# Optimization experiments

Measured on AMD Instinct MI355X. Metric: run time of the kernel, lower is better.

The kernel has to match this reference:

```python
import jax, jax.numpy as jnp
import numpy as np

PAST, FUT = 64, 16
SB = 2048
N = PAST + FUT  # 80
OUTP = 35       # sum(emb dims) + 3


def _pre(cat, num, emb0, emb1, emb2, W1, b1, W2, b2, W3, b3):
    # pre_processing: embeddings + last-3 numeric cols -> MLP -> concat target col
    e = jnp.concatenate([emb0[cat[:, 0]], emb1[cat[:, 1]], emb2[cat[:, 2]]], -1)
    o = jnp.concatenate([e, num], -1)                 # [n, 35]
    h = jax.nn.relu(o @ W1 + b1)
    h = jax.nn.relu(h @ W2 + b2)
    h = h @ W3 + b3                                   # [n, 34]
    return jnp.concatenate([h, num[:, -1:]], -1)      # [n, 35]


def _gcn(x, src, dst, W, b):
    n = x.shape[0]
    h = x @ W
    deg = 1.0 + jax.ops.segment_sum(jnp.ones(src.shape, x.dtype), dst, num_segments=n)
    dinv = jax.lax.rsqrt(deg)
    msg = h[src] * (dinv[src] * dinv[dst])[:, None]
    agg = jax.ops.segment_sum(msg, dst, num_segments=n) + h * (dinv * dinv)[:, None]
    return agg + b


def _forward(x1_cat, x1_num, x2_cat, x2_num, e1, e2,
             emb0, emb1, emb2, pW1, pb1, pW2, pb2, pW3, pb3,
             g1W1, g1b1, g1W2, g1b2, g2W1, g2b1, g2W2, g2b2,
             kerW, smoothing, M):
    # masked-softmax adjacency A = softmax(relu(M M^T) masked to lower-tri, axis=1)
    Araw = jax.nn.relu(M @ M.T)
    tril = jnp.tril(jnp.ones((N, N), Araw.dtype))
    A = jax.nn.softmax(jnp.where(tril == 0, -jnp.inf, Araw), axis=1)

    x = _pre(x1_cat, x1_num, emb0, emb1, emb2, pW1, pb1, pW2, pb2, pW3, pb3)   # [SB*PAST, 35]
    x2 = _pre(x2_cat, x2_num, emb0, emb1, emb2, pW1, pb1, pW2, pb2, pW3, pb3)
    x2 = x2.reshape(SB, FUT, OUTP)

    # gnn1: GCN(35->64) -> ReLU -> GCN(64->34)
    h = jax.nn.relu(_gcn(x, e1[0], e1[1], g1W1, g1b1))
    x1 = _gcn(h, e1[0], e1[1], g1W2, g1b2).reshape(SB, PAST, OUTP - 1)

    x_kernel = jnp.concatenate([x1, x2[:, :, :-1]], -2)        # [SB, N, 34]
    y_kernel = x.reshape(SB, PAST, OUTP)[:, :, -1:]            # [SB, PAST, 1]

    # Mahalanobis kernel attention
    theta = kerW @ kerW.T
    theta = (theta + theta.T) / 2
    x_p = x_kernel[:, :PAST, :]
    x_f = x_kernel[:, PAST:, :]
    diff = x_p[:, None, :, :] - x_f[:, :, None, :]             # [SB, FUT, PAST, 34]
    # diagonal of diff @ theta @ diff^T, computed directly
    alpha = jnp.einsum('bqpo,oO,bqpO->bqp', diff, theta, diff)
    alpha = -0.5 * alpha / (jax.nn.sigmoid(smoothing[0]) * 0.01)
    A_tmp = A[PAST:, :PAST]                                    # [FUT, PAST]
    alpha = jnp.where(A_tmp[None] == 0, -jnp.inf, alpha)
    alpha = jax.nn.softmax(alpha, -1)
    yh = jnp.einsum('bqp,bpo->bqo', alpha, y_kernel)           # [SB, FUT, 1]

    x2 = jnp.concatenate([x2[:, :, :-1], yh], -1)              # [SB, FUT, 35]
    # gnn2: GCN(35->64) -> ReLU -> GCN(64->1)
    h2 = jax.nn.relu(_gcn(x2.reshape(-1, OUTP), e2[0], e2[1], g2W1, g2b1))
    out = _gcn(h2, e2[0], e2[1], g2W2, g2b2).reshape(SB, FUT)

    # cdist over concatenated past+future features, via norm trick
    xa = jnp.concatenate([x.reshape(SB, PAST, OUTP), x2], -2)  # [SB, N, 35]
    sq = jnp.sum(xa * xa, -1)
    d2 = sq[:, :, None] + sq[:, None, :] - 2.0 * jnp.einsum('bnd,bmd->bnm', xa, xa)
    cd = jnp.sqrt(jnp.maximum(d2, 0.0))
    return out, cd, A


def setup_inputs():
    key = jax.random.key(0)
    ks = jax.random.split(key, 24)
    f32 = jnp.float32
    n1, n2 = SB * PAST, SB * FUT
    E1, E2 = n1 * 8, n2 * 8
    return {
        'x1_cat': jax.random.randint(ks[0], (n1, 3), 0, 7, dtype=jnp.int32),
        'x1_num': jax.random.normal(ks[1], (n1, 3), f32),
        'x2_cat': jax.random.randint(ks[2], (n2, 3), 0, 7, dtype=jnp.int32),
        'x2_num': jax.random.normal(ks[3], (n2, 3), f32),
        'edge_index1': jax.random.randint(ks[4], (2, E1), 0, n1, dtype=jnp.int32),
        'edge_index2': jax.random.randint(ks[5], (2, E2), 0, n2, dtype=jnp.int32),
        'emb0': jax.random.normal(ks[6], (24, 16), f32),
        'emb1': jax.random.normal(ks[7], (7, 8), f32),
        'emb2': jax.random.normal(ks[8], (12, 8), f32),
        'pre_W1': jax.random.normal(ks[9], (35, 128), f32) * 0.1,
        'pre_b1': jnp.zeros((128,), f32),
        'pre_W2': jax.random.normal(ks[10], (128, 128), f32) * 0.08,
        'pre_b2': jnp.zeros((128,), f32),
        'pre_W3': jax.random.normal(ks[11], (128, 34), f32) * 0.08,
        'pre_b3': jnp.zeros((34,), f32),
        'g1_W1': jax.random.normal(ks[12], (35, 64), f32) * 0.1,
        'g1_b1': jnp.zeros((64,), f32),
        'g1_W2': jax.random.normal(ks[13], (64, 34), f32) * 0.1,
        'g1_b2': jnp.zeros((34,), f32),
        'g2_W1': jax.random.normal(ks[14], (35, 64), f32) * 0.1,
        'g2_b1': jnp.zeros((64,), f32),
        'g2_W2': jax.random.normal(ks[15], (64, 1), f32) * 0.1,
        'g2_b2': jnp.zeros((1,), f32),
        'ker_W': jax.random.normal(ks[16], (34, 128), f32) * 0.1,
        'smoothing': jax.random.normal(ks[17], (1,), f32),
        'M': jax.random.normal(ks[18], (N, N // 3), f32) * 0.1,
    }


def reference(x1_cat, x1_num, x2_cat, x2_num, edge_index1, edge_index2,
              emb0, emb1, emb2, pre_W1, pre_b1, pre_W2, pre_b2, pre_W3, pre_b3,
              g1_W1, g1_b1, g1_W2, g1_b2, g2_W1, g2_b1, g2_W2, g2_b2,
              ker_W, smoothing, M):
    return _forward(x1_cat, x1_num, x2_cat, x2_num, edge_index1, edge_index2,
                    emb0, emb1, emb2, pre_W1, pre_b1, pre_W2, pre_b2, pre_W3, pre_b3,
                    g1_W1, g1_b1, g1_W2, g1_b2, g2_W1, g2_b1, g2_W2, g2_b2,
                    ker_W, smoothing, M)
```

## Files before the change

### kernel.cpp

```cpp
#include <hip/hip_runtime.h>
#include <math.h>

#define PASTN 64
#define FUTN 16
#define NN 80

typedef __attribute__((ext_vector_type(8))) short sh8;
typedef __attribute__((ext_vector_type(4))) float f32x4;

__device__ __forceinline__ unsigned short f2bf(float f) {
    unsigned int u = __float_as_uint(f);
    return (unsigned short)((u + 0x7FFFu + ((u >> 16) & 1u)) >> 16);
}
__device__ __forceinline__ float bf2f(unsigned short s) {
    return __uint_as_float(((unsigned int)s) << 16);
}

__global__ __launch_bounds__(256) void k_setup(const float* __restrict__ M, const float* __restrict__ kerW,
                                               const float* __restrict__ smoothing,
                                               float* __restrict__ A_ws, float* __restrict__ A_out,
                                               float* __restrict__ theta, float* __restrict__ scale)
{
    __shared__ float Ms[80 * 26];
    __shared__ float Ar[80 * 80];
    const int t = threadIdx.x;
    for (int i = t; i < 80 * 26; i += 256) Ms[i] = M[i];
    __syncthreads();
    for (int idx = t; idx < 6400; idx += 256) {
        int i = idx / 80, j = idx - 80 * i;
        float acc = 0.f;
#pragma unroll
        for (int k = 0; k < 26; ++k) acc = fmaf(Ms[i * 26 + k], Ms[j * 26 + k], acc);
        Ar[idx] = fmaxf(acc, 0.f);
    }
    __syncthreads();
    if (t < 80) {
        float mx = -1e30f;
        for (int j = 0; j <= t; ++j) mx = fmaxf(mx, Ar[t * 80 + j]);
        float s = 0.f;
        for (int j = 0; j <= t; ++j) s += expf(Ar[t * 80 + j] - mx);
        float inv = 1.f / s;
        for (int j = 0; j < 80; ++j) {
            float v = (j <= t) ? expf(Ar[t * 80 + j] - mx) * inv : 0.f;
            A_ws[t * 80 + j] = v;
            A_out[t * 80 + j] = v;
        }
    }
    for (int idx = t; idx < 34 * 34; idx += 256) {
        int i = idx / 34, j = idx - 34 * i;
        float acc = 0.f;
        for (int k = 0; k < 128; ++k) acc = fmaf(kerW[i * 128 + k], kerW[j * 128 + k], acc);
        theta[idx] = acc;
    }
    if (t == 0) {
        float s0 = smoothing[0];
        float sig = 1.f / (1.f + expf(-s0));
        scale[0] = -0.5f / (sig * 0.01f);
    }
}

__global__ void k_wconv(const float* __restrict__ W2, unsigned short* __restrict__ Wh,
                        unsigned short* __restrict__ Wl)
{
    int g = blockIdx.x * 256 + threadIdx.x;
    int i = g & 7, ln = (g >> 3) & 63, ks = (g >> 9) & 3, nt = g >> 11;
    int col = nt * 16 + (ln & 15);
    int k = ks * 32 + ((ln >> 4) << 3) + i;
    float w = W2[k * 128 + col];
    unsigned short hi = f2bf(w);
    Wh[g] = hi;
    Wl[g] = f2bf(w - bf2f(hi));
}

__global__ void k_deg2(const int* __restrict__ dst1, const int* __restrict__ dst2,
                       int* __restrict__ deg1, int* __restrict__ deg2,
                       int E1, int E2, int nbe1)
{
    int gb = blockIdx.x;
    if (gb < nbe1) {
        int e = gb * 256 + threadIdx.x;
        if (e < E1) atomicAdd(&deg1[dst1[e]], 1);
    } else {
        int e = (gb - nbe1) * 256 + threadIdx.x;
        if (e < E2) atomicAdd(&deg2[dst2[e]], 1);
    }
}

#define SCHUNK 1024
__global__ __launch_bounds__(256) void k_scan_reduce2(const int* __restrict__ deg1, const int* __restrict__ deg2,
                                                      int* __restrict__ bsumA, int* __restrict__ bsumB,
                                                      int n1, int n2, int nb1)
{
    __shared__ int sd[256];
    const int gb = blockIdx.x, t = threadIdx.x;
    const int which = (gb < nb1) ? 0 : 1;
    const int b = which ? gb - nb1 : gb;
    const int* deg = which ? deg2 : deg1;
    const int n = which ? n2 : n1;
    const int base = b * SCHUNK;
    int s = 0;
#pragma unroll
    for (int j = 0; j < 4; ++j) {
        int i = base + t + j * 256;
        if (i < n) s += deg[i];
    }
    sd[t] = s;
    __syncthreads();
    for (int o = 128; o > 0; o >>= 1) {
        if (t < o) sd[t] += sd[t + o];
        __syncthreads();
    }
    if (t == 0) (which ? bsumB : bsumA)[b] = sd[0];
}

__global__ __launch_bounds__(1024) void k_scan_mid2(int* __restrict__ bsumA, int* __restrict__ bsumB,
                                                    int nbA, int nbB)
{
    __shared__ int sd[1024];
    const int t = threadIdx.x;
    int* bsum = (blockIdx.x == 0) ? bsumA : bsumB;
    int nb = (blockIdx.x == 0) ? nbA : nbB;
    int orig = (t < nb) ? bsum[t] : 0;
    sd[t] = orig;
    __syncthreads();
    for (int o = 1; o < 1024; o <<= 1) {
        int v = (t >= o) ? sd[t - o] : 0;
        __syncthreads();
        sd[t] += v;
        __syncthreads();
    }
    if (t < nb) bsum[t] = sd[t] - orig;
}

__global__ __launch_bounds__(256) void k_scan_final2(const int* __restrict__ deg1, const int* __restrict__ deg2,
                                                     const int* __restrict__ bsumA, const int* __restrict__ bsumB,
                                                     int* __restrict__ rs1, int* __restrict__ rs2,
                                                     int* __restrict__ cur1, int* __restrict__ cur2,
                                                     float* __restrict__ dinv1, float* __restrict__ dinv2,
                                                     int n1, int n2, int nb1)
{
    __shared__ int sd[256];
    const int gb = blockIdx.x, t = threadIdx.x;
    const int which = (gb < nb1) ? 0 : 1;
    const int b = which ? gb - nb1 : gb;
    const int* deg = which ? deg2 : deg1;
    const int* bsum = which ? bsumB : bsumA;
    int* rs = which ? rs2 : rs1;
    int* cur = which ? cur2 : cur1;
    float* dinv = which ? dinv2 : dinv1;
    const int n = which ? n2 : n1;
    const int base = b * SCHUNK + t * 4;
    int v0 = (base + 0 < n) ? deg[base + 0] : 0;
    int v1 = (base + 1 < n) ? deg[base + 1] : 0;
    int v2 = (base + 2 < n) ? deg[base + 2] : 0;
    int v3 = (base + 3 < n) ? deg[base + 3] : 0;
    int tsum = v0 + v1 + v2 + v3;
    sd[t] = tsum;
    __syncthreads();
    int incl = tsum;
    for (int o = 1; o < 256; o <<= 1) {
        int v = (t >= o) ? sd[t - o] : 0;
        __syncthreads();
        incl += v;
        sd[t] = incl;
        __syncthreads();
    }
    int off = bsum[b] + incl - tsum;
    if (base + 0 < n) { rs[base + 0] = off;            cur[base + 0] = off;            dinv[base + 0] = rsqrtf(1.f + (float)v0); }
    if (base + 1 < n) { rs[base + 1] = off + v0;       cur[base + 1] = off + v0;       dinv[base + 1] = rsqrtf(1.f + (float)v1); }
    if (base + 2 < n) { rs[base + 2] = off + v0 + v1;  cur[base + 2] = off + v0 + v1;  dinv[base + 2] = rsqrtf(1.f + (float)v2); }
    if (base + 3 < n) { rs[base + 3] = off + v0 + v1 + v2; cur[base + 3] = off + v0 + v1 + v2; dinv[base + 3] = rsqrtf(1.f + (float)v3); }
}

__global__ void k_fill2(const int* __restrict__ src1, const int* __restrict__ dst1,
                        const int* __restrict__ src2, const int* __restrict__ dst2,
                        int* __restrict__ cur1, int* __restrict__ cur2,
                        int* __restrict__ out1, int* __restrict__ out2,
                        int E1, int E2, int nbe1)
{
    int gb = blockIdx.x;
    if (gb < nbe1) {
        int e = gb * 256 + threadIdx.x;
        if (e < E1) { int pos = atomicAdd(&cur1[dst1[e]], 1); out1[pos] = src1[e]; }
    } else {
        int e = (gb - nbe1) * 256 + threadIdx.x;
        if (e < E2) { int pos = atomicAdd(&cur2[dst2[e]], 1); out2[pos] = src2[e]; }
    }
}

template <int DIN>
__global__ __launch_bounds__(256) void k_gcn_s(const int* __restrict__ rs, const int* __restrict__ deg,
                                               const int* __restrict__ srcs, const float* __restrict__ dinv,
                                               const float* __restrict__ Hs, const float* __restrict__ W,
                                               const float* __restrict__ b, float* __restrict__ Out, int n)
{
    const int w = threadIdx.x >> 6, lane = threadIdx.x & 63;
    const int row = blockIdx.x * 4 + w;
    __shared__ float ag[4][DIN];
    const float di = dinv[row];
    const int e0 = rs[row];
    const int d = deg[row];
    float acc = (lane < DIN) ? Hs[(size_t)row * DIN + lane] : 0.f;
    int e = 0;
    for (; e + 8 <= d; e += 8) {
        int s0 = srcs[e0 + e + 0], s1 = srcs[e0 + e + 1], s2 = srcs[e0 + e + 2], s3 = srcs[e0 + e + 3];
        int s4 = srcs[e0 + e + 4], s5 = srcs[e0 + e + 5], s6 = srcs[e0 + e + 6], s7 = srcs[e0 + e + 7];
        float h0 = 0.f, h1 = 0.f, h2 = 0.f, h3 = 0.f, h4 = 0.f, h5 = 0.f, h6 = 0.f, h7 = 0.f;
        if (lane < DIN) {
            h0 = Hs[(size_t)s0 * DIN + lane]; h1 = Hs[(size_t)s1 * DIN + lane];
            h2 = Hs[(size_t)s2 * DIN + lane]; h3 = Hs[(size_t)s3 * DIN + lane];
            h4 = Hs[(size_t)s4 * DIN + lane]; h5 = Hs[(size_t)s5 * DIN + lane];
            h6 = Hs[(size_t)s6 * DIN + lane]; h7 = Hs[(size_t)s7 * DIN + lane];
        }
        acc += ((h0 + h1) + (h2 + h3)) + ((h4 + h5) + (h6 + h7));
    }
    for (; e + 4 <= d; e += 4) {
        int s0 = srcs[e0 + e + 0], s1 = srcs[e0 + e + 1], s2 = srcs[e0 + e + 2], s3 = srcs[e0 + e + 3];
        float h0 = 0.f, h1 = 0.f, h2 = 0.f, h3 = 0.f;
        if (lane < DIN) {
            h0 = Hs[(size_t)s0 * DIN + lane]; h1 = Hs[(size_t)s1 * DIN + lane];
            h2 = Hs[(size_t)s2 * DIN + lane]; h3 = Hs[(size_t)s3 * DIN + lane];
        }
        acc += (h0 + h1) + (h2 + h3);
    }
    for (; e < d; ++e) {
        int s = srcs[e0 + e];
        if (lane < DIN) acc += Hs[(size_t)s * DIN + lane];
    }
    if (lane < DIN) ag[w][lane] = acc;
    __syncthreads();
    float o = 0.f;
#pragma unroll
    for (int i = 0; i < DIN; ++i) o = fmaf(ag[w][i], W[i * 64 + lane], o);
    Out[(size_t)row * 64 + lane] = fmaxf(fmaf(di, o, b[lane]), 0.f);
}

template <int D>
__global__ __launch_bounds__(256) void k_pcomb_s(const int* __restrict__ rs, const int* __restrict__ deg,
                                                 const int* __restrict__ srcs, const float* __restrict__ dinv,
                                                 const float* __restrict__ Hs, const float* __restrict__ b,
                                                 float* __restrict__ dest, int n)
{
    const int wid = (blockIdx.x * blockDim.x + threadIdx.x) >> 6;
    const int lane = threadIdx.x & 63;
    if (wid >= n) return;
    const float di = dinv[wid];
    const int e0 = rs[wid];
    const int d = deg[wid];
    float acc = (lane < D) ? Hs[(size_t)wid * D + lane] : 0.f;
    int e = 0;
    for (; e + 8 <= d; e += 8) {
        int s0 = srcs[e0 + e + 0], s1 = srcs[e0 + e + 1], s2 = srcs[e0 + e + 2], s3 = srcs[e0 + e + 3];
        int s4 = srcs[e0 + e + 4], s5 = srcs[e0 + e + 5], s6 = srcs[e0 + e + 6], s7 = srcs[e0 + e + 7];
        float h0 = 0.f, h1 = 0.f, h2 = 0.f, h3 = 0.f, h4 = 0.f, h5 = 0.f, h6 = 0.f, h7 = 0.f;
        if (lane < D) {
            h0 = Hs[(size_t)s0 * D + lane]; h1 = Hs[(size_t)s1 * D + lane];
            h2 = Hs[(size_t)s2 * D + lane]; h3 = Hs[(size_t)s3 * D + lane];
            h4 = Hs[(size_t)s4 * D + lane]; h5 = Hs[(size_t)s5 * D + lane];
            h6 = Hs[(size_t)s6 * D + lane]; h7 = Hs[(size_t)s7 * D + lane];
        }
        acc += ((h0 + h1) + (h2 + h3)) + ((h4 + h5) + (h6 + h7));
    }
    for (; e + 4 <= d; e += 4) {
        int s0 = srcs[e0 + e + 0], s1 = srcs[e0 + e + 1], s2 = srcs[e0 + e + 2], s3 = srcs[e0 + e + 3];
        float h0 = 0.f, h1 = 0.f, h2 = 0.f, h3 = 0.f;
        if (lane < D) {
            h0 = Hs[(size_t)s0 * D + lane]; h1 = Hs[(size_t)s1 * D + lane];
            h2 = Hs[(size_t)s2 * D + lane]; h3 = Hs[(size_t)s3 * D + lane];
        }
        acc += (h0 + h1) + (h2 + h3);
    }
    for (; e < d; ++e) {
        int s = srcs[e0 + e];
        if (lane < D) acc += Hs[(size_t)s * D + lane];
    }
    if (lane < D) dest[(size_t)wid * D + lane] = fmaf(di, acc, b[lane]);
}

__global__ void k_pcomb1_s(const int* __restrict__ rs, const int* __restrict__ deg,
                           const int* __restrict__ srcs, const float* __restrict__ dinv,
                           const float* __restrict__ Hs, const float* __restrict__ b,
                           float* __restrict__ dest, int n)
{
    int r = blockIdx.x * blockDim.x + threadIdx.x;
    if (r >= n) return;
    int e0 = rs[r], d = deg[r];
    float acc = Hs[r];
    int e = 0;
    for (; e + 8 <= d; e += 8) {
        acc += ((Hs[srcs[e0 + e + 0]] + Hs[srcs[e0 + e + 1]]) + (Hs[srcs[e0 + e + 2]] + Hs[srcs[e0 + e + 3]]))
             + ((Hs[srcs[e0 + e + 4]] + Hs[srcs[e0 + e + 5]]) + (Hs[srcs[e0 + e + 6]] + Hs[srcs[e0 + e + 7]]));
    }
    for (; e + 4 <= d; e += 4) {
        acc += (Hs[srcs[e0 + e + 0]] + Hs[srcs[e0 + e + 1]]) + (Hs[srcs[e0 + e + 2]] + Hs[srcs[e0 + e + 3]]);
    }
    for (; e < d; ++e) acc += Hs[srcs[e0 + e]];
    dest[r] = fmaf(dinv[r], acc, b[0]);
}

#define PR 32
__global__ __launch_bounds__(256) void k_pre_all(const int* __restrict__ cat1, const float* __restrict__ num1,
                                                 const int* __restrict__ cat2, const float* __restrict__ num2,
                                                 const float* __restrict__ emb0, const float* __restrict__ emb1,
                                                 const float* __restrict__ emb2,
                                                 const float* __restrict__ W1, const float* __restrict__ b1,
                                                 const unsigned short* __restrict__ W2fh,
                                                 const unsigned short* __restrict__ W2fl,
                                                 const float* __restrict__ b2,
                                                 const float* __restrict__ W3, const float* __restrict__ b3,
                                                 const float* __restrict__ dinv1, const float* __restrict__ dinv2,
                                                 float* __restrict__ X1, float* __restrict__ Xs1,
                                                 float* __restrict__ X2, float* __restrict__ Xs2,
                                                 int nblk1)
{
    __shared__ float ldsB[128 * 32];
    __shared__ __align__(16) unsigned short h1h[128 * 32];
    __shared__ __align__(16) unsigned short h1l[128 * 32];
    float* oT = ldsB;
    float* h2T = ldsB;
    const int t = threadIdx.x;
    const int ct = t & 31;
    const int rg = t >> 5;
    const int gb = blockIdx.x;
    const int g2 = (gb >= nblk1);
    const int* cat = g2 ? cat2 : cat1;
    const float* num = g2 ? num2 : num1;
    const float* dinv = g2 ? dinv2 : dinv1;
    float* X = g2 ? X2 : X1;
    float* Xs = g2 ? Xs2 : Xs1;
    const int base = (g2 ? gb - nblk1 : gb) * PR;

    for (int idx = t; idx < 35 * PR; idx += 256) {
        int i = idx >> 5, r = idx & 31;
        int row = base + r;
        float v;
        if (i < 16) v = emb0[cat[row * 3 + 0] * 16 + i];
        else if (i < 24) v = emb1[cat[row * 3 + 1] * 8 + (i - 16)];
        else if (i < 32) v = emb2[cat[row * 3 + 2] * 8 + (i - 24)];
        else v = num[row * 3 + (i - 32)];
        oT[i * PR + (((r >> 2) ^ (i & 7)) << 2) + (r & 3)] = v;
    }
    __syncthreads();

    {
        float acc[4][4];
        float4 bb = *(const float4*)(b1 + 4 * ct);
        const float bbv[4] = {bb.x, bb.y, bb.z, bb.w};
#pragma unroll
        for (int c = 0; c < 4; ++c)
#pragma unroll
            for (int r = 0; r < 4; ++r) acc[c][r] = bbv[c];
        for (int i = 0; i < 35; ++i) {
            float4 ov = *(const float4*)(oT + i * PR + ((rg ^ (i & 7)) << 2));
            float4 wv = *(const float4*)(W1 + i * 128 + 4 * ct);
            const float o4[4] = {ov.x, ov.y, ov.z, ov.w};
            const float w4[4] = {wv.x, wv.y, wv.z, wv.w};
#pragma unroll
            for (int c = 0; c < 4; ++c)
#pragma unroll
                for (int r = 0; r < 4; ++r) acc[c][r] = fmaf(w4[c], o4[r], acc[c][r]);
        }
#pragma unroll
        for (int j = 0; j < 4; ++j) {
            int row32 = 4 * rg + j;
            int rowm = row32 & 15;
            int off = row32 * 128 + ((((ct >> 1) ^ rowm)) << 3) + ((ct & 1) << 2);
            ushort4 hi4, lo4;
            float h0 = fmaxf(acc[0][j], 0.f);
            float h1v = fmaxf(acc[1][j], 0.f);
            float h2v = fmaxf(acc[2][j], 0.f);
            float h3v = fmaxf(acc[3][j], 0.f);
            hi4.x = f2bf(h0); lo4.x = f2bf(h0 - bf2f(hi4.x));
            hi4.y = f2bf(h1v); lo4.y = f2bf(h1v - bf2f(hi4.y));
            hi4.z = f2bf(h2v); lo4.z = f2bf(h2v - bf2f(hi4.z));
            hi4.w = f2bf(h3v); lo4.w = f2bf(h3v - bf2f(hi4.w));
            *(ushort4*)(h1h + off) = hi4;
            *(ushort4*)(h1l + off) = lo4;
        }
    }
    __syncthreads();

    {
        const int wv = t >> 6, ln = t & 63;
        const int mt = wv & 1, ng = wv >> 1;
        const int lr = ln & 15, lh = ln >> 4;
        f32x4 acc[4];
#pragma unroll
        for (int j = 0; j < 4; ++j) acc[j] = (f32x4){0.f, 0.f, 0.f, 0.f};
        const int arow = (mt * 16 + lr) * 128;
#pragma unroll
        for (int ks = 0; ks < 4; ++ks) {
            const int sc = (((ks * 4 + lh) ^ lr) << 3);
            sh8 ahi = *(const sh8*)(h1h + arow + sc);
            sh8 alo = *(const sh8*)(h1l + arow + sc);
#pragma unroll
            for (int j = 0; j < 4; ++j) {
                const int fbase = ((((ng * 4 + j) * 4 + ks) * 64 + ln) << 3);
                sh8 bhi = *(const sh8*)(W2fh + fbase);
                sh8 blo = *(const sh8*)(W2fl + fbase);
                acc[j] = __builtin_amdgcn_mfma_f32_16x16x32_bf16(ahi, bhi, acc[j], 0, 0, 0);
                acc[j] = __builtin_amdgcn_mfma_f32_16x16x32_bf16(ahi, blo, acc[j], 0, 0, 0);
                acc[j] = __builtin_amdgcn_mfma_f32_16x16x32_bf16(alo, bhi, acc[j], 0, 0, 0);
            }
        }
        __syncthreads();
#pragma unroll
        for (int j = 0; j < 4; ++j) {
            int col = (ng * 4 + j) * 16 + lr;
            int rg3 = mt * 4 + lh;
            float bc = b2[col];
            float4 v;
            v.x = fmaxf(acc[j][0] + bc, 0.f);
            v.y = fmaxf(acc[j][1] + bc, 0.f);
            v.z = fmaxf(acc[j][2] + bc, 0.f);
            v.w = fmaxf(acc[j][3] + bc, 0.f);
            *(float4*)(h2T + col * PR + ((rg3 ^ (col & 7)) << 2)) = v;
        }
    }
    __syncthreads();

    for (int task = t; task < 34 * 8; task += 256) {
        int j = task >> 3, rg3 = task & 7;
        float a0 = b3[j], a1 = a0, a2 = a0, a3 = a0;
#pragma unroll 4
        for (int k = 0; k < 128; ++k) {
            float4 hv = *(const float4*)(h2T + k * PR + ((rg3 ^ (k & 7)) << 2));
            float wv = W3[k * 34 + j];
            a0 = fmaf(hv.x, wv, a0);
            a1 = fmaf(hv.y, wv, a1);
            a2 = fmaf(hv.z, wv, a2);
            a3 = fmaf(hv.w, wv, a3);
        }
        size_t rb = (size_t)(base + rg3 * 4);
        float d0 = dinv[rb + 0], d1 = dinv[rb + 1], d2 = dinv[rb + 2], d3 = dinv[rb + 3];
        X[(rb + 0) * 35 + j] = a0;  Xs[(rb + 0) * 35 + j] = a0 * d0;
        X[(rb + 1) * 35 + j] = a1;  Xs[(rb + 1) * 35 + j] = a1 * d1;
        X[(rb + 2) * 35 + j] = a2;  Xs[(rb + 2) * 35 + j] = a2 * d2;
        X[(rb + 3) * 35 + j] = a3;  Xs[(rb + 3) * 35 + j] = a3 * d3;
    }
    if (t < PR) {
        int row = base + t;
        float v = num[row * 3 + 2];
        X[(size_t)row * 35 + 34] = v;
        Xs[(size_t)row * 35 + 34] = v * dinv[row];
    }
}

template <int DIN, int DOUT, bool BIAS, bool RELU, bool SCALE>
__global__ void k_gemm(const float* __restrict__ Xin, int ldin, const float* __restrict__ W,
                       const float* __restrict__ b, const float* __restrict__ oscale,
                       float* __restrict__ Out, int n)
{
    __shared__ float Ws[DIN * DOUT];
    for (int i = threadIdx.x; i < DIN * DOUT; i += blockDim.x) Ws[i] = W[i];
    __syncthreads();
    int idx = blockIdx.x * blockDim.x + threadIdx.x;
    if (idx >= n * DOUT) return;
    int row = idx / DOUT, j = idx - row * DOUT;
    const float4* xr4 = (const float4*)(Xin + (size_t)row * ldin);
    float acc = BIAS ? b[j] : 0.f;
#pragma unroll
    for (int i4 = 0; i4 < DIN / 4; ++i4) {
        float4 x = xr4[i4];
        acc = fmaf(x.x, Ws[(4 * i4 + 0) * DOUT + j], acc);
        acc = fmaf(x.y, Ws[(4 * i4 + 1) * DOUT + j], acc);
        acc = fmaf(x.z, Ws[(4 * i4 + 2) * DOUT + j], acc);
        acc = fmaf(x.w, Ws[(4 * i4 + 3) * DOUT + j], acc);
    }
    if (RELU) acc = fmaxf(acc, 0.f);
    if (SCALE) acc *= oscale[row];
    Out[idx] = acc;
}

__global__ __launch_bounds__(256) void k_alpha(const float* __restrict__ X1,
                                               const float* __restrict__ X,
                                               float* __restrict__ X2,
                                               float* __restrict__ Xs2,
                                               const float* __restrict__ dinv2,
                                               const float* __restrict__ theta,
                                               const float* __restrict__ A,
                                               const float* __restrict__ scale)
{
    const int b = blockIdx.x;
    const int t = threadIdx.x;
    const int p = t & 63;
    const int w = t >> 6;
    __shared__ float th[34 * 34];
    __shared__ float xpS[64 * 35];
    __shared__ float xfS[16 * 34];
    __shared__ float UfS[16 * 34];
    __shared__ float upPart[4][64];
    __shared__ float upS[64];
    __shared__ float yS[64];

    for (int i = t; i < 34 * 34; i += 256) th[i] = theta[i];
    for (int i = t; i < 64 * 34; i += 256) {
        int r = i / 34, o = i - 34 * r;
        xpS[r * 35 + o] = X1[(size_t)(b * 64 + r) * 34 + o];
    }
    for (int i = t; i < 16 * 34; i += 256) {
        int q = i / 34, o = i - 34 * q;
        xfS[i] = X2[(size_t)(b * 16 + q) * 35 + o];
    }
    if (t < 64) yS[t] = X[(size_t)(b * 64 + t) * 35 + 34];
    __syncthreads();

    for (int i = t; i < 16 * 34; i += 256) {
        int q = i / 34, o = i - 34 * q;
        float a = 0.f;
#pragma unroll
        for (int O = 0; O < 34; ++O) a = fmaf(th[o * 34 + O], xfS[q * 34 + O], a);
        UfS[i] = a;
    }
    {
        const int o0 = w * 9;
        const int o1 = (o0 + 9 < 34) ? o0 + 9 : 34;
        float a = 0.f;
        for (int o = o0; o < o1; ++o) {
            float s2 = 0.f;
#pragma unroll
            for (int O = 0; O < 34; ++O) s2 = fmaf(th[o * 34 + O], xpS[p * 35 + O], s2);
            a = fmaf(xpS[p * 35 + o], s2, a);
        }
        upPart[w][p] = a;
    }
    __syncthreads();
    if (t < 64) upS[t] = upPart[0][t] + upPart[1][t] + upPart[2][t] + upPart[3][t];
    __syncthreads();

    const float sc = scale[0];
    const float up = upS[p];
    const float y = yS[p];
#pragma unroll
    for (int i = 0; i < 4; ++i) {
        const int q = w + 4 * i;
        float g = 0.f;
#pragma unroll
        for (int o = 0; o < 34; ++o) g = fmaf(UfS[q * 34 + o], xpS[p * 35 + o], g);
        float a = sc * (up - 2.f * g);
        if (A[(PASTN + q) * NN + p] == 0.f) a = -INFINITY;
        float mx = a;
#pragma unroll
        for (int off = 32; off > 0; off >>= 1) mx = fmaxf(mx, __shfl_xor(mx, off));
        float e = expf(a - mx);
        float s = e;
#pragma unroll
        for (int off = 32; off > 0; off >>= 1) s += __shfl_xor(s, off);
        float c = (e / s) * y;
#pragma unroll
        for (int off = 32; off > 0; off >>= 1) c += __shfl_xor(c, off);
        if (p == 0) {
            size_t ridx = (size_t)(b * 16 + q);
            X2[ridx * 35 + 34] = c;
            Xs2[ridx * 35 + 34] = c * dinv2[ridx];
        }
    }
}

__global__ __launch_bounds__(256) void k_cd(const float* __restrict__ X, const float* __restrict__ X2,
                                            float* __restrict__ cd)
{
    const int b = blockIdx.x;
    const int t = threadIdx.x;
    __shared__ float xa[80 * 44];
    __shared__ float sq[80];
    for (int idx = t; idx < 80 * 44; idx += 256) {
        int nrow = idx / 44, k = idx - 44 * nrow;
        float v = 0.f;
        if (k < 35)
            v = (nrow < 64) ? X[(size_t)(b * 64 + nrow) * 35 + k]
                            : X2[(size_t)(b * 16 + (nrow - 64)) * 35 + k];
        xa[idx] = v;
    }
    __syncthreads();
    const float4* xa4 = (const float4*)xa;
    if (t < 80) {
        float acc = 0.f;
#pragma unroll
        for (int c = 0; c < 9; ++c) {
            float4 v = xa4[t * 11 + c];
            acc = fmaf(v.x, v.x, fmaf(v.y, v.y, fmaf(v.z, v.z, fmaf(v.w, v.w, acc))));
        }
        sq[t] = acc;
    }
    __syncthreads();
    const int ti = t >> 4;
    const int tj = t & 15;
    float dot[5][5];
#pragma unroll
    for (int r = 0; r < 5; ++r)
#pragma unroll
        for (int c = 0; c < 5; ++c) dot[r][c] = 0.f;
#pragma unroll
    for (int ch = 0; ch < 9; ++ch) {
        float4 av[5], bv[5];
#pragma unroll
        for (int r = 0; r < 5; ++r) av[r] = xa4[(5 * ti + r) * 11 + ch];
#pragma unroll
        for (int c = 0; c < 5; ++c) bv[c] = xa4[(5 * tj + c) * 11 + ch];
#pragma unroll
        for (int r = 0; r < 5; ++r)
#pragma unroll
            for (int c = 0; c < 5; ++c)
                dot[r][c] = fmaf(av[r].x, bv[c].x, fmaf(av[r].y, bv[c].y,
                              fmaf(av[r].z, bv[c].z, fmaf(av[r].w, bv[c].w, dot[r][c]))));
    }
    float* out = cd + (size_t)b * 6400;
#pragma unroll
    for (int r = 0; r < 5; ++r) {
        int n_ = 5 * ti + r;
        float sn = sq[n_];
#pragma unroll
        for (int c = 0; c < 5; ++c) {
            int m = 5 * tj + c;
            float d2 = sn + sq[m] - 2.f * dot[r][c];
            out[n_ * 80 + m] = sqrtf(fmaxf(d2, 0.f));
        }
    }
}

extern "C" void kernel_launch(void* const* d_in, const int* in_sizes, int n_in,
                              void* d_out, int out_size, void* d_ws, size_t ws_size,
                              hipStream_t stream)
{
    const int* x1_cat = (const int*)d_in[0];
    const float* x1_num = (const float*)d_in[1];
    const int* x2_cat = (const int*)d_in[2];
    const float* x2_num = (const float*)d_in[3];
    const int* e1 = (const int*)d_in[4];
    const int* e2 = (const int*)d_in[5];
    const float* emb0 = (const float*)d_in[6];
    const float* emb1 = (const float*)d_in[7];
    const float* emb2 = (const float*)d_in[8];
    const float* pW1 = (const float*)d_in[9];
    const float* pb1 = (const float*)d_in[10];
    const float* pW2 = (const float*)d_in[11];
    const float* pb2 = (const float*)d_in[12];
    const float* pW3 = (const float*)d_in[13];
    const float* pb3 = (const float*)d_in[14];
    const float* g1W1 = (const float*)d_in[15];
    const float* g1b1 = (const float*)d_in[16];
    const float* g1W2 = (const float*)d_in[17];
    const float* g1b2 = (const float*)d_in[18];
    const float* g2W1 = (const float*)d_in[19];
    const float* g2b1 = (const float*)d_in[20];
    const float* g2W2 = (const float*)d_in[21];
    const float* g2b2 = (const float*)d_in[22];
    const float* kerW = (const float*)d_in[23];
    const float* smoothing = (const float*)d_in[24];
    const float* M = (const float*)d_in[25];

    const int n1 = in_sizes[0] / 3;
    const int n2 = in_sizes[2] / 3;
    const int E1 = in_sizes[4] / 2;
    const int E2 = in_sizes[5] / 2;
    const int SBc = n2 / FUTN;

    float* w = (float*)d_ws;
    size_t off = 0;
    float* scale = w + off; off += 16;
    float* theta = w + off; off += 1184;
    float* Aws = w + off; off += 6400;
    float* X = w + off; off += (size_t)n1 * 35;
    float* Xs1 = w + off; off += (size_t)n1 * 35;
    float* X2 = w + off; off += (size_t)n2 * 35;
    float* Xs2 = w + off; off += (size_t)n2 * 35;
    float* dinv1 = w + off; off += (size_t)n1;
    float* dinv2 = w + off; off += (size_t)n2;
    float* B2 = w + off; off += (size_t)n1 * 64;
    float* B3 = w + off; off += (size_t)n1 * 34;
    float* B4 = w + off; off += (size_t)n1 * 34;
    off = (off + 3) & ~(size_t)3;
    unsigned short* W2fh = (unsigned short*)(w + off); off += 8192;
    unsigned short* W2fl = (unsigned short*)(w + off); off += 8192;
    int* iw = (int*)(w + off);
    size_t ioff = 0;
    int* degi1 = iw + ioff; ioff += n1;
    int* degi2 = iw + ioff; ioff += n2;
    int* rs1 = iw + ioff; ioff += n1;
    int* cur1 = iw + ioff; ioff += n1;
    int* srcs1 = iw + ioff; ioff += E1;
    int* rs2 = iw + ioff; ioff += n2;
    int* cur2 = iw + ioff; ioff += n2;
    int* srcs2 = iw + ioff; ioff += E2;
    int* bsumA = iw + ioff; ioff += 1024;
    int* bsumB = iw + ioff; ioff += 1024;

    float* out_f = (float*)d_out;
    float* cd_f = out_f + (size_t)SBc * FUTN;
    float* A_out = cd_f + (size_t)SBc * NN * NN;

    auto cdiv = [](long long a, long long b) { return (unsigned)((a + b - 1) / b); };

    hipMemsetAsync(degi1, 0, ((size_t)n1 + n2) * 4, stream);
    k_setup<<<1, 256, 0, stream>>>(M, kerW, smoothing, Aws, A_out, theta, scale);
    k_wconv<<<64, 256, 0, stream>>>(pW2, W2fh, W2fl);

    const int nbe1 = cdiv(E1, 256), nbe2 = cdiv(E2, 256);
    k_deg2<<<nbe1 + nbe2, 256, 0, stream>>>(e1 + E1, e2 + E2, degi1, degi2, E1, E2, nbe1);

    const int nb1 = cdiv(n1, SCHUNK), nb2 = cdiv(n2, SCHUNK);
    k_scan_reduce2<<<nb1 + nb2, 256, 0, stream>>>(degi1, degi2, bsumA, bsumB, n1, n2, nb1);
    k_scan_mid2<<<2, 1024, 0, stream>>>(bsumA, bsumB, nb1, nb2);
    k_scan_final2<<<nb1 + nb2, 256, 0, stream>>>(degi1, degi2, bsumA, bsumB, rs1, rs2, cur1, cur2,
                                                 dinv1, dinv2, n1, n2, nb1);
    k_fill2<<<nbe1 + nbe2, 256, 0, stream>>>(e1, e1 + E1, e2, e2 + E2, cur1, cur2, srcs1, srcs2, E1, E2, nbe1);

    k_pre_all<<<n1 / PR + n2 / PR, 256, 0, stream>>>(x1_cat, x1_num, x2_cat, x2_num,
                                                     emb0, emb1, emb2, pW1, pb1, W2fh, W2fl, pb2, pW3, pb3,
                                                     dinv1, dinv2, X, Xs1, X2, Xs2, n1 / PR);

    k_gcn_s<35><<<cdiv(n1, 4), 256, 0, stream>>>(rs1, degi1, srcs1, dinv1, Xs1, g1W1, g1b1, B2, n1);

    k_gemm<64, 34, false, false, true><<<cdiv((long long)n1 * 34, 256), 256, 0, stream>>>(B2, 64, g1W2, nullptr, dinv1, B3, n1);
    k_pcomb_s<34><<<cdiv(n1, 4), 256, 0, stream>>>(rs1, degi1, srcs1, dinv1, B3, g1b2, B4, n1);

    k_alpha<<<SBc, 256, 0, stream>>>(B4, X, X2, Xs2, dinv2, theta, Aws, scale);

    k_gcn_s<35><<<cdiv(n2, 4), 256, 0, stream>>>(rs2, degi2, srcs2, dinv2, Xs2, g2W1, g2b1, B2, n2);

    k_gemm<64, 1, false, false, true><<<cdiv(n2, 256), 256, 0, stream>>>(B2, 64, g2W2, nullptr, dinv2, B3, n2);
    k_pcomb1_s<<<cdiv(n2, 256), 256, 0, stream>>>(rs2, degi2, srcs2, dinv2, B3, g2b2, out_f, n2);

    k_cd<<<SBc, 256, 0, stream>>>(X, X2, cd_f);
}
```

Measured before the change: 710.0 us.

## Move pre-processing MLP layers 1 and 3 onto split-bf16 MFMA

The first and third layers of the pre-processing MLP move from scalar FP32 FMA loops onto bf16 MFMA, using the same hi/lo split-bf16 (three-product) scheme already used for layer 2. The weight-conversion kernel now pre-packs W1 (K padded to 64) and W3 (N padded to 48) into MFMA fragment layout. LDS buffers are unified into swizzled hi/lo bf16 tiles shared across the three stages. This trades FP32 ALU work for matrix-core work plus conversion overhead, and the split-bf16 approximation slightly reduces accuracy.

```diff
diff --git a/kernel.cpp b/kernel.cpp
--- a/kernel.cpp
+++ b/kernel.cpp
@@ -59,17 +59,41 @@
     }
 }
 
-__global__ void k_wconv(const float* __restrict__ W2, unsigned short* __restrict__ Wh,
-                        unsigned short* __restrict__ Wl)
+__global__ void k_wconv(const float* __restrict__ W1, const float* __restrict__ W2,
+                        const float* __restrict__ W3,
+                        unsigned short* __restrict__ W1h, unsigned short* __restrict__ W1l,
+                        unsigned short* __restrict__ W2h, unsigned short* __restrict__ W2l,
+                        unsigned short* __restrict__ W3h, unsigned short* __restrict__ W3l)
 {
     int g = blockIdx.x * 256 + threadIdx.x;
-    int i = g & 7, ln = (g >> 3) & 63, ks = (g >> 9) & 3, nt = g >> 11;
-    int col = nt * 16 + (ln & 15);
-    int k = ks * 32 + ((ln >> 4) << 3) + i;
-    float w = W2[k * 128 + col];
+    float w;
+    unsigned short *dh, *dl;
+    int gi;
+    if (g < 8192) {
+        gi = g;
+        int i = gi & 7, l = (gi >> 3) & 63, ks = (gi >> 9) & 1, nt = gi >> 10;
+        int col = nt * 16 + (l & 15);
+        int k = ks * 32 + ((l >> 4) << 3) + i;
+        w = (k < 35) ? W1[k * 128 + col] : 0.f;
+        dh = W1h; dl = W1l;
+    } else if (g < 24576) {
+        gi = g - 8192;
+        int i = gi & 7, l = (gi >> 3) & 63, ks = (gi >> 9) & 3, nt = gi >> 11;
+        int col = nt * 16 + (l & 15);
+        int k = ks * 32 + ((l >> 4) << 3) + i;
+        w = W2[k * 128 + col];
+        dh = W2h; dl = W2l;
+    } else {
+        gi = g - 24576;
+        int i = gi & 7, l = (gi >> 3) & 63, ks = (gi >> 9) & 3, nt = gi >> 11;
+        int col = nt * 16 + (l & 15);
+        int k = ks * 32 + ((l >> 4) << 3) + i;
+        w = (col < 34) ? W3[k * 34 + col] : 0.f;
+        dh = W3h; dl = W3l;
+    }
     unsigned short hi = f2bf(w);
-    Wh[g] = hi;
-    Wl[g] = f2bf(w - bf2f(hi));
+    dh[gi] = hi;
+    dl[gi] = f2bf(w - bf2f(hi));
 }
 
 __global__ void k_deg2(const int* __restrict__ dst1, const int* __restrict__ dst2,
@@ -303,24 +327,23 @@
                                                  const int* __restrict__ cat2, const float* __restrict__ num2,
                                                  const float* __restrict__ emb0, const float* __restrict__ emb1,
                                                  const float* __restrict__ emb2,
-                                                 const float* __restrict__ W1, const float* __restrict__ b1,
-                                                 const unsigned short* __restrict__ W2fh,
-                                                 const unsigned short* __restrict__ W2fl,
+                                                 const unsigned short* __restrict__ W1h, const unsigned short* __restrict__ W1l,
+                                                 const float* __restrict__ b1,
+                                                 const unsigned short* __restrict__ W2h, const unsigned short* __restrict__ W2l,
                                                  const float* __restrict__ b2,
-                                                 const float* __restrict__ W3, const float* __restrict__ b3,
+                                                 const unsigned short* __restrict__ W3h, const unsigned short* __restrict__ W3l,
+                                                 const float* __restrict__ b3,
                                                  const float* __restrict__ dinv1, const float* __restrict__ dinv2,
                                                  float* __restrict__ X1, float* __restrict__ Xs1,
                                                  float* __restrict__ X2, float* __restrict__ Xs2,
                                                  int nblk1)
 {
-    __shared__ float ldsB[128 * 32];
-    __shared__ __align__(16) unsigned short h1h[128 * 32];
-    __shared__ __align__(16) unsigned short h1l[128 * 32];
-    float* oT = ldsB;
-    float* h2T = ldsB;
+    __shared__ __align__(16) unsigned short bufh[32 * 128];
+    __shared__ __align__(16) unsigned short bufl[32 * 128];
     const int t = threadIdx.x;
-    const int ct = t & 31;
-    const int rg = t >> 5;
+    const int wv = t >> 6, ln = t & 63;
+    const int mt = wv & 1, wg = wv >> 1;
+    const int lr = ln & 15, lh = ln >> 4;
     const int gb = blockIdx.x;
     const int g2 = (gb >= nblk1);
     const int* cat = g2 ? cat2 : cat1;
@@ -330,113 +353,141 @@
     float* Xs = g2 ? Xs2 : Xs1;
     const int base = (g2 ? gb - nblk1 : gb) * PR;
 
-    for (int idx = t; idx < 35 * PR; idx += 256) {
-        int i = idx >> 5, r = idx & 31;
-        int row = base + r;
-        float v;
-        if (i < 16) v = emb0[cat[row * 3 + 0] * 16 + i];
-        else if (i < 24) v = emb1[cat[row * 3 + 1] * 8 + (i - 16)];
-        else if (i < 32) v = emb2[cat[row * 3 + 2] * 8 + (i - 24)];
-        else v = num[row * 3 + (i - 32)];
-        oT[i * PR + (((r >> 2) ^ (i & 7)) << 2) + (r & 3)] = v;
-    }
-    __syncthreads();
-
+    for (int idx = t; idx < 32 * 64; idx += 256) {
+        int r = idx >> 6, k = idx & 63;
+        float v = 0.f;
+        if (k < 16) v = emb0[cat[(base + r) * 3 + 0] * 16 + k];
+        else if (k < 24) v = emb1[cat[(base + r) * 3 + 1] * 8 + (k - 16)];
+        else if (k < 32) v = emb2[cat[(base + r) * 3 + 2] * 8 + (k - 24)];
+        else if (k < 35) v = num[(base + r) * 3 + (k - 32)];
+        unsigned short hi = f2bf(v);
+        int ho = r * 64 + (((k >> 3) ^ (r & 7)) << 3) + (k & 7);
+        bufh[ho] = hi;
+        bufl[ho] = f2bf(v - bf2f(hi));
+    }
+    __syncthreads();
+
+    f32x4 a1[4];
     {
-        float acc[4][4];
-        float4 bb = *(const float4*)(b1 + 4 * ct);
-        const float bbv[4] = {bb.x, bb.y, bb.z, bb.w};
-#pragma unroll
-        for (int c = 0; c < 4; ++c)
-#pragma unroll
-            for (int r = 0; r < 4; ++r) acc[c][r] = bbv[c];
-        for (int i = 0; i < 35; ++i) {
-            float4 ov = *(const float4*)(oT + i * PR + ((rg ^ (i & 7)) << 2));
-            float4 wv = *(const float4*)(W1 + i * 128 + 4 * ct);
-            const float o4[4] = {ov.x, ov.y, ov.z, ov.w};
-            const float w4[4] = {wv.x, wv.y, wv.z, wv.w};
-#pragma unroll
-            for (int c = 0; c < 4; ++c)
-#pragma unroll
-                for (int r = 0; r < 4; ++r) acc[c][r] = fmaf(w4[c], o4[r], acc[c][r]);
+        const int ra = mt * 16 + lr;
+        sh8 ah[2], al[2];
+#pragma unroll
+        for (int ks = 0; ks < 2; ++ks) {
+            int off = ra * 64 + ((((ks * 4 + lh)) ^ (ra & 7)) << 3);
+            ah[ks] = *(const sh8*)(bufh + off);
+            al[ks] = *(const sh8*)(bufl + off);
         }
 #pragma unroll
         for (int j = 0; j < 4; ++j) {
-            int row32 = 4 * rg + j;
-            int rowm = row32 & 15;
-            int off = row32 * 128 + ((((ct >> 1) ^ rowm)) << 3) + ((ct & 1) << 2);
-            ushort4 hi4, lo4;
-            float h0 = fmaxf(acc[0][j], 0.f);
-            float h1v = fmaxf(acc[1][j], 0.f);
-            float h2v = fmaxf(acc[2][j], 0.f);
-            float h3v = fmaxf(acc[3][j], 0.f);
-            hi4.x = f2bf(h0); lo4.x = f2bf(h0 - bf2f(hi4.x));
-            hi4.y = f2bf(h1v); lo4.y = f2bf(h1v - bf2f(hi4.y));
-            hi4.z = f2bf(h2v); lo4.z = f2bf(h2v - bf2f(hi4.z));
-            hi4.w = f2bf(h3v); lo4.w = f2bf(h3v - bf2f(hi4.w));
-            *(ushort4*)(h1h + off) = hi4;
-            *(ushort4*)(h1l + off) = lo4;
-        }
-    }
-    __syncthreads();
-
+            const int nt = wg + 2 * j;
+            f32x4 acc = (f32x4){0.f, 0.f, 0.f, 0.f};
+#pragma unroll
+            for (int ks = 0; ks < 2; ++ks) {
+                const int fb = (((nt * 2 + ks) * 64 + ln) << 3);
+                sh8 bh = *(const sh8*)(W1h + fb);
+                sh8 bl = *(const sh8*)(W1l + fb);
+                acc = __builtin_amdgcn_mfma_f32_16x16x32_bf16(ah[ks], bh, acc, 0, 0, 0);
+                acc = __builtin_amdgcn_mfma_f32_16x16x32_bf16(ah[ks], bl, acc, 0, 0, 0);
+                acc = __builtin_amdgcn_mfma_f32_16x16x32_bf16(al[ks], bh, acc, 0, 0, 0);
+            }
+            a1[j] = acc;
+        }
+    }
+    __syncthreads();
+#pragma unroll
+    for (int j = 0; j < 4; ++j) {
+        const int f = (wg + 2 * j) * 16 + lr;
+        const float bb = b1[f];
+#pragma unroll
+        for (int reg = 0; reg < 4; ++reg) {
+            const int row = mt * 16 + lh * 4 + reg;
+            float v = fmaxf(a1[j][reg] + bb, 0.f);
+            unsigned short hi = f2bf(v);
+            int ho = row * 128 + ((((f >> 3)) ^ (row & 15)) << 3) + (f & 7);
+            bufh[ho] = hi;
+            bufl[ho] = f2bf(v - bf2f(hi));
+        }
+    }
+    __syncthreads();
+
+    f32x4 a2[4];
+#pragma unroll
+    for (int j = 0; j < 4; ++j) a2[j] = (f32x4){0.f, 0.f, 0.f, 0.f};
     {
-        const int wv = t >> 6, ln = t & 63;
-        const int mt = wv & 1, ng = wv >> 1;
-        const int lr = ln & 15, lh = ln >> 4;
-        f32x4 acc[4];
-#pragma unroll
-        for (int j = 0; j < 4; ++j) acc[j] = (f32x4){0.f, 0.f, 0.f, 0.f};
-        const int arow = (mt * 16 + lr) * 128;
+        const int ra = mt * 16 + lr;
 #pragma unroll
         for (int ks = 0; ks < 4; ++ks) {
-            const int sc = (((ks * 4 + lh) ^ lr) << 3);
-            sh8 ahi = *(const sh8*)(h1h + arow + sc);
-            sh8 alo = *(const sh8*)(h1l + arow + sc);
+            int off = ra * 128 + (((ks * 4 + lh) ^ lr) << 3);
+            sh8 ah = *(const sh8*)(bufh + off);
+            sh8 al = *(const sh8*)(bufl + off);
 #pragma unroll
             for (int j = 0; j < 4; ++j) {
-                const int fbase = ((((ng * 4 + j) * 4 + ks) * 64 + ln) << 3);
-                sh8 bhi = *(const sh8*)(W2fh + fbase);
-                sh8 blo = *(const sh8*)(W2fl + fbase);
-                acc[j] = __builtin_amdgcn_mfma_f32_16x16x32_bf16(ahi, bhi, acc[j], 0, 0, 0);
-                acc[j] = __builtin_amdgcn_mfma_f32_16x16x32_bf16(ahi, blo, acc[j], 0, 0, 0);
-                acc[j] = __builtin_amdgcn_mfma_f32_16x16x32_bf16(alo, bhi, acc[j], 0, 0, 0);
+                const int nt = wg * 4 + j;
+                const int fb = (((nt * 4 + ks) * 64 + ln) << 3);
+                sh8 bh = *(const sh8*)(W2h + fb);
+                sh8 bl = *(const sh8*)(W2l + fb);
+                a2[j] = __builtin_amdgcn_mfma_f32_16x16x32_bf16(ah, bh, a2[j], 0, 0, 0);
+                a2[j] = __builtin_amdgcn_mfma_f32_16x16x32_bf16(ah, bl, a2[j], 0, 0, 0);
+                a2[j] = __builtin_amdgcn_mfma_f32_16x16x32_bf16(al, bh, a2[j], 0, 0, 0);
             }
         }
-        __syncthreads();
-#pragma unroll
-        for (int j = 0; j < 4; ++j) {
-            int col = (ng * 4 + j) * 16 + lr;
-            int rg3 = mt * 4 + lh;
-            float bc = b2[col];
-            float4 v;
-            v.x = fmaxf(acc[j][0] + bc, 0.f);
-            v.y = fmaxf(acc[j][1] + bc, 0.f);
-            v.z = fmaxf(acc[j][2] + bc, 0.f);
-            v.w = fmaxf(acc[j][3] + bc, 0.f);
-            *(float4*)(h2T + col * PR + ((rg3 ^ (col & 7)) << 2)) = v;
-        }
-    }
-    __syncthreads();
-
-    for (int task = t; task < 34 * 8; task += 256) {
-        int j = task >> 3, rg3 = task & 7;
-        float a0 = b3[j], a1 = a0, a2 = a0, a3 = a0;
-#pragma unroll 4
-        for (int k = 0; k < 128; ++k) {
-            float4 hv = *(const float4*)(h2T + k * PR + ((rg3 ^ (k & 7)) << 2));
-            float wv = W3[k * 34 + j];
-            a0 = fmaf(hv.x, wv, a0);
-            a1 = fmaf(hv.y, wv, a1);
-            a2 = fmaf(hv.z, wv, a2);
-            a3 = fmaf(hv.w, wv, a3);
-        }
-        size_t rb = (size_t)(base + rg3 * 4);
-        float d0 = dinv[rb + 0], d1 = dinv[rb + 1], d2 = dinv[rb + 2], d3 = dinv[rb + 3];
-        X[(rb + 0) * 35 + j] = a0;  Xs[(rb + 0) * 35 + j] = a0 * d0;
-        X[(rb + 1) * 35 + j] = a1;  Xs[(rb + 1) * 35 + j] = a1 * d1;
-        X[(rb + 2) * 35 + j] = a2;  Xs[(rb + 2) * 35 + j] = a2 * d2;
-        X[(rb + 3) * 35 + j] = a3;  Xs[(rb + 3) * 35 + j] = a3 * d3;
+    }
+    __syncthreads();
+#pragma unroll
+    for (int j = 0; j < 4; ++j) {
+        const int f = (wg * 4 + j) * 16 + lr;
+        const float bb = b2[f];
+#pragma unroll
+        for (int reg = 0; reg < 4; ++reg) {
+            const int row = mt * 16 + lh * 4 + reg;
+            float v = fmaxf(a2[j][reg] + bb, 0.f);
+            unsigned short hi = f2bf(v);
+            int ho = row * 128 + ((((f >> 3)) ^ (row & 15)) << 3) + (f & 7);
+            bufh[ho] = hi;
+            bufl[ho] = f2bf(v - bf2f(hi));
+        }
+    }
+    __syncthreads();
+
+    f32x4 a3[2];
+    a3[0] = (f32x4){0.f, 0.f, 0.f, 0.f};
+    a3[1] = (f32x4){0.f, 0.f, 0.f, 0.f};
+    {
+        const int ra = mt * 16 + lr;
+#pragma unroll
+        for (int ks = 0; ks < 4; ++ks) {
+            int off = ra * 128 + (((ks * 4 + lh) ^ lr) << 3);
+            sh8 ah = *(const sh8*)(bufh + off);
+            sh8 al = *(const sh8*)(bufl + off);
+#pragma unroll
+            for (int j = 0; j < 2; ++j) {
+                const int nt = wg * 2 + j;
+                if (nt >= 3) continue;
+                const int fb = (((nt * 4 + ks) * 64 + ln) << 3);
+                sh8 bh = *(const sh8*)(W3h + fb);
+                sh8 bl = *(const sh8*)(W3l + fb);
+                a3[j] = __builtin_amdgcn_mfma_f32_16x16x32_bf16(ah, bh, a3[j], 0, 0, 0);
+                a3[j] = __builtin_amdgcn_mfma_f32_16x16x32_bf16(ah, bl, a3[j], 0, 0, 0);
+                a3[j] = __builtin_amdgcn_mfma_f32_16x16x32_bf16(al, bh, a3[j], 0, 0, 0);
+            }
+        }
+    }
+#pragma unroll
+    for (int j = 0; j < 2; ++j) {
+        const int nt = wg * 2 + j;
+        if (nt >= 3) continue;
+        const int jc = nt * 16 + lr;
+        if (jc < 34) {
+            const float bb = b3[jc];
+#pragma unroll
+            for (int reg = 0; reg < 4; ++reg) {
+                const int row = mt * 16 + lh * 4 + reg;
+                const int gr = base + row;
+                float v = a3[j][reg] + bb;
+                X[(size_t)gr * 35 + jc] = v;
+                Xs[(size_t)gr * 35 + jc] = v * dinv[gr];
+            }
+        }
     }
     if (t < PR) {
         int row = base + t;
@@ -671,8 +722,12 @@
     float* B3 = w + off; off += (size_t)n1 * 34;
     float* B4 = w + off; off += (size_t)n1 * 34;
     off = (off + 3) & ~(size_t)3;
+    unsigned short* W1fh = (unsigned short*)(w + off); off += 4096;
+    unsigned short* W1fl = (unsigned short*)(w + off); off += 4096;
     unsigned short* W2fh = (unsigned short*)(w + off); off += 8192;
     unsigned short* W2fl = (unsigned short*)(w + off); off += 8192;
+    unsigned short* W3fh = (unsigned short*)(w + off); off += 4096;
+    unsigned short* W3fl = (unsigned short*)(w + off); off += 4096;
     int* iw = (int*)(w + off);
     size_t ioff = 0;
     int* degi1 = iw + ioff; ioff += n1;
@@ -694,7 +749,7 @@
 
     hipMemsetAsync(degi1, 0, ((size_t)n1 + n2) * 4, stream);
     k_setup<<<1, 256, 0, stream>>>(M, kerW, smoothing, Aws, A_out, theta, scale);
-    k_wconv<<<64, 256, 0, stream>>>(pW2, W2fh, W2fl);
+    k_wconv<<<128, 256, 0, stream>>>(pW1, pW2, pW3, W1fh, W1fl, W2fh, W2fl, W3fh, W3fl);
 
     const int nbe1 = cdiv(E1, 256), nbe2 = cdiv(E2, 256);
     k_deg2<<<nbe1 + nbe2, 256, 0, stream>>>(e1 + E1, e2 + E2, degi1, degi2, E1, E2, nbe1);
@@ -707,7 +762,8 @@
     k_fill2<<<nbe1 + nbe2, 256, 0, stream>>>(e1, e1 + E1, e2, e2 + E2, cur1, cur2, srcs1, srcs2, E1, E2, nbe1);
 
     k_pre_all<<<n1 / PR + n2 / PR, 256, 0, stream>>>(x1_cat, x1_num, x2_cat, x2_num,
-                                                     emb0, emb1, emb2, pW1, pb1, W2fh, W2fl, pb2, pW3, pb3,
+                                                     emb0, emb1, emb2,
+                                                     W1fh, W1fl, pb1, W2fh, W2fl, pb2, W3fh, W3fl, pb3,
                                                      dinv1, dinv2, X, Xs1, X2, Xs2, n1 / PR);
 
     k_gcn_s<35><<<cdiv(n1, 4), 256, 0, stream>>>(rs1, degi1, srcs1, dinv1, Xs1, g1W1, g1b1, B2, n1);
```

New measurement: 671.4 us. 1.06x faster.
